# Kernel tuning notes

Hardware: AMD Instinct MI355X
Metric: run time of the kernel (lower is better)

The kernel has to match this reference:

```python
import jax, jax.numpy as jnp
import numpy as np

C_M, C_Z, C, H = 256, 128, 32, 8
EPS = 1e-5

def _ln(x, g, b):
    mu = jnp.mean(x, axis=-1, keepdims=True)
    var = jnp.var(x, axis=-1, keepdims=True)
    return (x - mu) * jax.lax.rsqrt(var + EPS) * g + b

def setup_inputs() -> dict:
    key = jax.random.key(0)
    ks = jax.random.split(key, 12)
    s = 0.02
    return {
        "m": jax.random.normal(ks[0], (128, 384, C_M), jnp.float32),
        "z": jax.random.normal(ks[1], (384, 384, C_Z), jnp.float32),
        "ln_m_g": jnp.ones((C_M,), jnp.float32),
        "ln_m_b": jnp.zeros((C_M,), jnp.float32),
        "ln_z_g": jnp.ones((C_Z,), jnp.float32),
        "ln_z_b": jnp.zeros((C_Z,), jnp.float32),
        "Wq": jax.random.normal(ks[2], (C_M, H, C), jnp.float32) * s,
        "Wk": jax.random.normal(ks[3], (C_M, H, C), jnp.float32) * s,
        "Wv": jax.random.normal(ks[4], (C_M, H, C), jnp.float32) * s,
        "Wb": jax.random.normal(ks[5], (C_Z, H), jnp.float32) * s,
        "Wg": jax.random.normal(ks[6], (C_M, H, C), jnp.float32) * s,
        "bg": jnp.ones((H, C), jnp.float32),
        "Wo": jax.random.normal(ks[7], (H, C, C_M), jnp.float32) * s,
        "bo": jnp.zeros((C_M,), jnp.float32),
    }

def reference(m, z, ln_m_g, ln_m_b, ln_z_g, ln_z_b, Wq, Wk, Wv, Wb, Wg, bg, Wo, bo):
    # Algorithm 7: MSA row-wise gated self-attention with pair bias.
    mn = _ln(m, ln_m_g, ln_m_b)                      # (S, R, c_m)
    zn = _ln(z, ln_z_g, ln_z_b)                      # (R, R, c_z)
    b = jnp.einsum('qkz,zh->hqk', zn, Wb)            # per-head pair bias (H, R, R)
    q = jnp.einsum('srm,mhc->shrc', mn, Wq)          # (S, H, R, C)
    k = jnp.einsum('srm,mhc->shrc', mn, Wk)
    v = jnp.einsum('srm,mhc->shrc', mn, Wv)
    logits = jnp.einsum('shqc,shkc->shqk', q, k) * (1.0 / np.sqrt(C)) + b[None]
    a = jax.nn.softmax(logits, axis=-1)              # (S, H, Rq, Rk)
    o = jnp.einsum('shqk,shkc->sqhc', a, v)          # (S, R, H, C)
    g = jax.nn.sigmoid(jnp.einsum('srm,mhc->srhc', mn, Wg) + bg)
    o = g * o
    out = jnp.einsum('srhc,hcm->srm', o, Wo) + bo    # (S, R, c_m)
    return out
```

## Files before the change

kernel.cpp:

```cpp
#include <hip/hip_runtime.h>
#include <hip/hip_bf16.h>

#define DEVINL __device__ __forceinline__

typedef __attribute__((ext_vector_type(8))) short bf16x8;
typedef __attribute__((ext_vector_type(4))) float f32x4;

DEVINL float bf2f(unsigned short u) {
    unsigned int v = ((unsigned int)u) << 16;
    return __builtin_bit_cast(float, v);
}
DEVINL unsigned short f2bf(float f) {
    unsigned int u = __builtin_bit_cast(unsigned int, f);
    u = (u + 0x7FFFu + ((u >> 16) & 1u)) >> 16;
    return (unsigned short)u;
}
DEVINL float wave_sum(float v) {
#pragma unroll
    for (int off = 32; off > 0; off >>= 1) v += __shfl_xor(v, off, 64);
    return v;
}
DEVINL void gload16(const void* g, void* l) {
    __builtin_amdgcn_global_load_lds(
        (const __attribute__((address_space(1))) void*)g,
        (__attribute__((address_space(3))) void*)l, 16, 0, 0);
}


__global__ __launch_bounds__(256) void k_ln_m(const float* __restrict__ m,
                                              const float* __restrict__ gm,
                                              const float* __restrict__ bm,
                                              unsigned short* __restrict__ mn) {
    const int lane = threadIdx.x & 63;
    const int row  = (blockIdx.x << 2) + (threadIdx.x >> 6);
    const float4 x = *(const float4*)(m + (size_t)row * 256 + lane * 4);
    float s  = x.x + x.y + x.z + x.w;
    float s2 = x.x * x.x + x.y * x.y + x.z * x.z + x.w * x.w;
    s = wave_sum(s); s2 = wave_sum(s2);
    const float mean = s * (1.f / 256.f);
    const float var  = s2 * (1.f / 256.f) - mean * mean;
    const float rstd = rsqrtf(var + 1e-5f);
    const float4 g = *(const float4*)(gm + lane * 4);
    const float4 b = *(const float4*)(bm + lane * 4);
    ushort4 o;
    o.x = f2bf((x.x - mean) * rstd * g.x + b.x);
    o.y = f2bf((x.y - mean) * rstd * g.y + b.y);
    o.z = f2bf((x.z - mean) * rstd * g.z + b.z);
    o.w = f2bf((x.w - mean) * rstd * g.w + b.w);
    *(ushort4*)(mn + (size_t)row * 256 + lane * 4) = o;
}

__global__ __launch_bounds__(64) void k_prep_wb(const float* __restrict__ gz,
                                                const float* __restrict__ bz,
                                                const float* __restrict__ Wb,
                                                float* __restrict__ W2,
                                                float* __restrict__ SK) {
    const int lane = threadIdx.x;
    const float LOG2E = 1.4426950408889634f;
    float sC[8], sK[8];
#pragma unroll
    for (int h = 0; h < 8; h++) { sC[h] = 0.f; sK[h] = 0.f; }
#pragma unroll
    for (int i = 0; i < 2; i++) {
        const int c = lane + i * 64;
        const float g = gz[c] * LOG2E, b = bz[c] * LOG2E;
        const float4 w0 = *(const float4*)(Wb + c * 8);
        const float4 w1 = *(const float4*)(Wb + c * 8 + 4);
        const float w[8] = {w0.x, w0.y, w0.z, w0.w, w1.x, w1.y, w1.z, w1.w};
        float wg[8];
#pragma unroll
        for (int h = 0; h < 8; h++) {
            wg[h] = g * w[h];
            sC[h] += wg[h];
            sK[h] += b * w[h];
        }
        float4 o0 = {wg[0], wg[1], wg[2], wg[3]};
        float4 o1 = {wg[4], wg[5], wg[6], wg[7]};
        *(float4*)(W2 + c * 8)     = o0;
        *(float4*)(W2 + c * 8 + 4) = o1;
    }
#pragma unroll
    for (int h = 0; h < 8; h++) { sC[h] = wave_sum(sC[h]); sK[h] = wave_sum(sK[h]); }
    if (lane == 0) {
#pragma unroll
        for (int h = 0; h < 8; h++) { SK[h] = sC[h]; SK[8 + h] = sK[h]; }
    }
}

__global__ __launch_bounds__(256) void k_ln_z_bias(const float* __restrict__ z,
                                                   const float* __restrict__ W2,
                                                   const float* __restrict__ SK,
                                                   float* __restrict__ bT) {
    const int p = blockIdx.x * 256 + threadIdx.x;
    const float* zp = z + (size_t)p * 128;

    float d[8];
#pragma unroll
    for (int h = 0; h < 8; h++) d[h] = 0.f;
    float s = 0.f, s2 = 0.f;

#pragma unroll 8
    for (int cq = 0; cq < 32; cq++) {
        const float4 zv = *(const float4*)(zp + cq * 4);
        const float za[4] = {zv.x, zv.y, zv.z, zv.w};
        s  += (zv.x + zv.y) + (zv.z + zv.w);
        s2 += (zv.x * zv.x + zv.y * zv.y) + (zv.z * zv.z + zv.w * zv.w);
#pragma unroll
        for (int cc = 0; cc < 4; cc++) {
            const float* w = W2 + (cq * 4 + cc) * 8;
#pragma unroll
            for (int h = 0; h < 8; h++) d[h] += za[cc] * w[h];
        }
    }

    const float mean = s * (1.f / 128.f);
    const float var  = s2 * (1.f / 128.f) - mean * mean;
    const float rstd = rsqrtf(var + 1e-5f);
    const float rm   = rstd * mean;

    const int q  = p / 384;
    const int kk = p - q * 384;
    const int kb = kk >> 5, kk5 = kk & 31;
    const size_t o = ((size_t)((kb * 2 + ((kk5 >> 2) & 1)) * 4 + (kk5 >> 3)) * 384 + q) * 4 + (kk5 & 3);
    float* bp = bT + o;
#pragma unroll
    for (int h = 0; h < 8; h++)
        bp[(size_t)h * 147456] = rstd * d[h] - rm * SK[h] + SK[8 + h];
}

__global__ __launch_bounds__(256) void k_prep(const float* __restrict__ S,
                                              unsigned short* __restrict__ D) {
    __shared__ float T[64][68];
    const int k0 = blockIdx.x * 64, n0 = blockIdx.y * 64;
    const int tr = threadIdx.x >> 4, tc4 = (threadIdx.x & 15) * 4;
#pragma unroll
    for (int i = 0; i < 4; i++) {
        const int k = i * 16 + tr;
        const float4 v = *(const float4*)(S + (size_t)(k0 + k) * 256 + n0 + tc4);
        T[k][tc4 + 0] = v.x; T[k][tc4 + 1] = v.y; T[k][tc4 + 2] = v.z; T[k][tc4 + 3] = v.w;
    }
    __syncthreads();
#pragma unroll
    for (int i = 0; i < 4; i++) {
        const int n = i * 16 + tr;
        ushort4 o;
        o.x = f2bf(T[tc4 + 0][n]);
        o.y = f2bf(T[tc4 + 1][n]);
        o.z = f2bf(T[tc4 + 2][n]);
        o.w = f2bf(T[tc4 + 3][n]);
        *(ushort4*)(D + (size_t)(n0 + n) * 256 + k0 + tc4) = o;
    }
}

__global__ __launch_bounds__(256) void k_prep4(const float* __restrict__ Wq,
                                               const float* __restrict__ Wk,
                                               const float* __restrict__ Wv,
                                               const float* __restrict__ Wg,
                                               unsigned short* __restrict__ D) {
    __shared__ float T[64][68];
    const int zz = blockIdx.z;
    const float* S = (zz == 0) ? Wq : (zz == 1) ? Wk : (zz == 2) ? Wv : Wg;
    unsigned short* Dz = D + (size_t)zz * 65536;
    const int k0 = blockIdx.x * 64, n0 = blockIdx.y * 64;
    const int tr = threadIdx.x >> 4, tc4 = (threadIdx.x & 15) * 4;
#pragma unroll
    for (int i = 0; i < 4; i++) {
        const int k = i * 16 + tr;
        const float4 v = *(const float4*)(S + (size_t)(k0 + k) * 256 + n0 + tc4);
        T[k][tc4 + 0] = v.x; T[k][tc4 + 1] = v.y; T[k][tc4 + 2] = v.z; T[k][tc4 + 3] = v.w;
    }
    __syncthreads();
#pragma unroll
    for (int i = 0; i < 4; i++) {
        const int n = i * 16 + tr;
        ushort4 o;
        o.x = f2bf(T[tc4 + 0][n]);
        o.y = f2bf(T[tc4 + 1][n]);
        o.z = f2bf(T[tc4 + 2][n]);
        o.w = f2bf(T[tc4 + 3][n]);
        *(ushort4*)(Dz + (size_t)(n0 + n) * 256 + k0 + tc4) = o;
    }
}

template<int MODE>
__global__ __launch_bounds__(256) void k_gemm(const unsigned short* __restrict__ A,
                                              const unsigned short* __restrict__ BT,
                                              const float* __restrict__ bias,
                                              unsigned short* __restrict__ o0,
                                              unsigned short* __restrict__ o1,
                                              unsigned short* __restrict__ o2,
                                              unsigned short* __restrict__ o3,
                                              float* __restrict__ fout) {
    __shared__ unsigned short As[8192];
    __shared__ unsigned short Bs[8192];
    const int tid = threadIdx.x;
    const int w = tid >> 6, lane = tid & 63;
    const int col = lane & 15, quad = lane >> 4;
    const int wm = w >> 1, wn = w & 1;
    const int R0 = blockIdx.x * 128;
    const int N0 = blockIdx.y * 128;

    f32x4 acc[4][4];
#pragma unroll
    for (int i = 0; i < 4; i++)
#pragma unroll
        for (int j = 0; j < 4; j++) acc[i][j] = (f32x4){0.f, 0.f, 0.f, 0.f};

    const unsigned short* Ag = A  + (size_t)R0 * 256;
    const unsigned short* Bg = BT + (size_t)N0 * 256;

    for (int ks = 0; ks < 4; ks++) {
        if (ks) __syncthreads();
        const int k0 = ks * 64;
#pragma unroll
        for (int it = 0; it < 4; it++) {
            const int cb = it * 256 + w * 64;
            const int chunk = cb + lane;
            const int row = chunk >> 3;
            const int ch  = (chunk & 7) ^ (row & 7);
            gload16(Ag + (size_t)row * 256 + k0 + ch * 8, As + (size_t)cb * 8);
            gload16(Bg + (size_t)row * 256 + k0 + ch * 8, Bs + (size_t)cb * 8);
        }
        __syncthreads();
#pragma unroll
        for (int ksub = 0; ksub < 2; ksub++) {
            const int c = ksub * 4 + quad;
            bf16x8 Af[4], Bf[4];
#pragma unroll
            for (int mt = 0; mt < 4; mt++) {
                const int r = wm * 64 + mt * 16 + col;
                Af[mt] = *(const bf16x8*)(As + r * 64 + (c ^ (r & 7)) * 8);
            }
#pragma unroll
            for (int nt = 0; nt < 4; nt++) {
                const int r = wn * 64 + nt * 16 + col;
                Bf[nt] = *(const bf16x8*)(Bs + r * 64 + (c ^ (r & 7)) * 8);
            }
#pragma unroll
            for (int mt = 0; mt < 4; mt++)
#pragma unroll
                for (int nt = 0; nt < 4; nt++)
                    acc[mt][nt] = __builtin_amdgcn_mfma_f32_16x16x32_bf16(Af[mt], Bf[nt], acc[mt][nt], 0, 0, 0);
        }
    }

    if (MODE == 0) {
        const int mat = blockIdx.y >> 1;
        const int s = R0 / 384;
        const int rbase = R0 - s * 384;
        const int n0r = (blockIdx.y & 1) * 128;
        if (mat == 1 || mat == 2) {
            unsigned short* outp = (mat == 1) ? o1 : o2;
#pragma unroll
            for (int nt = 0; nt < 4; nt++) {
                const int hc = n0r + wn * 64 + nt * 16 + col;
                const int h = hc >> 5, cc = hc & 31;
                unsigned short* op = outp + (size_t)(s * 8 + h) * 12288;
                if (mat == 1) {
#pragma unroll
                    for (int mt = 0; mt < 4; mt++) {
                        const int r2 = rbase + wm * 64 + mt * 16 + quad * 4;
                        const int ab = (r2 >> 5) * 1024 + ((r2 >> 2) & 1) * 512
                                     + ((r2 & 31) >> 3) * 128 + cc;
#pragma unroll
                        for (int rr = 0; rr < 4; rr++)
                            op[ab + rr * 32] = f2bf(acc[mt][nt][rr]);
                    }
                } else {
                    unsigned short* opv = op + (cc >> 4) * 512 + (cc & 15) * 32;
#pragma unroll
                    for (int mt = 0; mt < 4; mt++) {
                        const int r2 = rbase + wm * 64 + mt * 16 + quad * 4;
                        ushort4 o;
                        o.x = f2bf(acc[mt][nt][0]);
                        o.y = f2bf(acc[mt][nt][1]);
                        o.z = f2bf(acc[mt][nt][2]);
                        o.w = f2bf(acc[mt][nt][3]);
                        *(ushort4*)(opv + (r2 >> 5) * 1024 + (r2 & 31)) = o;
                    }
                }
            }
        } else {
            unsigned short* outp = (mat == 0) ? o0 : o3;
#pragma unroll
            for (int nt = 0; nt < 4; nt++) {
                const int hc = n0r + wn * 64 + nt * 16 + col;
                const int h = hc >> 5, cc = hc & 31;
                const float bgv = bias[hc];
                unsigned short* op = outp + (size_t)(s * 8 + h) * 384 * 32 + cc;
#pragma unroll
                for (int mt = 0; mt < 4; mt++) {
                    const int r2 = rbase + wm * 64 + mt * 16 + quad * 4;
#pragma unroll
                    for (int rr = 0; rr < 4; rr++) {
                        float v = acc[mt][nt][rr];
                        v = (mat == 3) ? 1.f / (1.f + __expf(-(v + bgv)))
                                       : v * 0.25507788224f;
                        op[(size_t)(r2 + rr) * 32] = f2bf(v);
                    }
                }
            }
        }
    } else {
#pragma unroll
        for (int nt = 0; nt < 4; nt++) {
            const int n = N0 + wn * 64 + nt * 16 + col;
            const float bov = bias[n];
            float* op = fout + n;
#pragma unroll
            for (int mt = 0; mt < 4; mt++) {
                const int r2 = R0 + wm * 64 + mt * 16 + quad * 4;
#pragma unroll
                for (int rr = 0; rr < 4; rr++)
                    op[(size_t)(r2 + rr) * 256] = acc[mt][nt][rr] + bov;
            }
        }
    }
}

__global__ __launch_bounds__(256) void k_attn(const unsigned short* __restrict__ qw,
                                              const unsigned short* __restrict__ kf,
                                              const unsigned short* __restrict__ vf,
                                              const unsigned short* __restrict__ gw,
                                              const float* __restrict__ bT,
                                              unsigned short* __restrict__ og) {
    const int s    = blockIdx.x & 127;
    const int half = (blockIdx.x >> 7) & 1;
    const int h    = blockIdx.x >> 8;
    const int tid  = threadIdx.x;
    const int wave = tid >> 6;
    const int lane = tid & 63;
    const int col  = lane & 15;
    const int quad = lane >> 4;
    const size_t base = ((size_t)(s * 8 + h)) * 12288;
    const int qbase = half * 192 + wave * 48;

    bf16x8 Qf[3];
#pragma unroll
    for (int qt = 0; qt < 3; qt++)
        Qf[qt] = *(const bf16x8*)(qw + base + (size_t)(qbase + qt * 16 + col) * 32 + quad * 8);

    f32x4 OT0[3], OT1[3];
    float lsum[3];
#pragma unroll
    for (int qt = 0; qt < 3; qt++) {
        OT0[qt] = (f32x4){0.f, 0.f, 0.f, 0.f};
        OT1[qt] = (f32x4){0.f, 0.f, 0.f, 0.f};
        lsum[qt] = 0.f;
    }

    const unsigned short* kwb = kf + base + col * 32 + quad * 8;
    const unsigned short* vtb = vf + base + col * 32 + quad * 8;
    const float* bp = bT + (size_t)h * 147456 + ((size_t)quad * 384 + qbase + col) * 4;

    for (int kb = 0; kb < 12; kb++) {
        const bf16x8 Kf0 = *(const bf16x8*)(kwb);
        const bf16x8 Kf1 = *(const bf16x8*)(kwb + 512);
        const bf16x8 VA0 = *(const bf16x8*)(vtb);
        const bf16x8 VA1 = *(const bf16x8*)(vtb + 512);
        kwb += 1024; vtb += 1024;
        f32x4 B0[3], B1[3];
#pragma unroll
        for (int qt = 0; qt < 3; qt++) {
            const float4 a = *(const float4*)(bp + qt * 64);
            const float4 b = *(const float4*)(bp + 6144 + qt * 64);
            B0[qt] = (f32x4){a.x, a.y, a.z, a.w};
            B1[qt] = (f32x4){b.x, b.y, b.z, b.w};
        }
        bp += 12288;
#pragma unroll
        for (int qt = 0; qt < 3; qt++) {
            const f32x4 St0 = __builtin_amdgcn_mfma_f32_16x16x32_bf16(Kf0, Qf[qt], B0[qt], 0, 0, 0);
            const f32x4 St1 = __builtin_amdgcn_mfma_f32_16x16x32_bf16(Kf1, Qf[qt], B1[qt], 0, 0, 0);
            float p0[4], p1[4];
            p0[0] = __builtin_amdgcn_exp2f(St0[0]);
            p0[1] = __builtin_amdgcn_exp2f(St0[1]);
            p0[2] = __builtin_amdgcn_exp2f(St0[2]);
            p0[3] = __builtin_amdgcn_exp2f(St0[3]);
            p1[0] = __builtin_amdgcn_exp2f(St1[0]);
            p1[1] = __builtin_amdgcn_exp2f(St1[1]);
            p1[2] = __builtin_amdgcn_exp2f(St1[2]);
            p1[3] = __builtin_amdgcn_exp2f(St1[3]);
            lsum[qt] += (p0[0] + p0[1]) + (p0[2] + p0[3]) + (p1[0] + p1[1]) + (p1[2] + p1[3]);
            union { bf16x8 v; __hip_bfloat162 h2[4]; } U;
            U.h2[0] = __float22bfloat162_rn(make_float2(p0[0], p0[1]));
            U.h2[1] = __float22bfloat162_rn(make_float2(p0[2], p0[3]));
            U.h2[2] = __float22bfloat162_rn(make_float2(p1[0], p1[1]));
            U.h2[3] = __float22bfloat162_rn(make_float2(p1[2], p1[3]));
            OT0[qt] = __builtin_amdgcn_mfma_f32_16x16x32_bf16(VA0, U.v, OT0[qt], 0, 0, 0);
            OT1[qt] = __builtin_amdgcn_mfma_f32_16x16x32_bf16(VA1, U.v, OT1[qt], 0, 0, 0);
        }
    }

#pragma unroll
    for (int qt = 0; qt < 3; qt++) {
        float l = lsum[qt];
        l += __shfl_xor(l, 16, 64);
        l += __shfl_xor(l, 32, 64);
        const float inv = 1.f / l;
        const int q = qbase + qt * 16 + col;
        const ushort4 g0 = *(const ushort4*)(gw + base + (size_t)q * 32 + quad * 4);
        const ushort4 g1 = *(const ushort4*)(gw + base + (size_t)q * 32 + quad * 4 + 16);
        ushort4 o0s, o1s;
        o0s.x = f2bf(OT0[qt][0] * inv * bf2f(g0.x));
        o0s.y = f2bf(OT0[qt][1] * inv * bf2f(g0.y));
        o0s.z = f2bf(OT0[qt][2] * inv * bf2f(g0.z));
        o0s.w = f2bf(OT0[qt][3] * inv * bf2f(g0.w));
        o1s.x = f2bf(OT1[qt][0] * inv * bf2f(g1.x));
        o1s.y = f2bf(OT1[qt][1] * inv * bf2f(g1.y));
        o1s.z = f2bf(OT1[qt][2] * inv * bf2f(g1.z));
        o1s.w = f2bf(OT1[qt][3] * inv * bf2f(g1.w));
        unsigned short* op = og + ((size_t)s * 384 + q) * 256 + h * 32 + quad * 4;
        *(ushort4*)(op)      = o0s;
        *(ushort4*)(op + 16) = o1s;
    }
}

extern "C" void kernel_launch(void* const* d_in, const int* in_sizes, int n_in,
                              void* d_out, int out_size, void* d_ws, size_t ws_size,
                              hipStream_t stream) {
    const float* m   = (const float*)d_in[0];
    const float* z   = (const float*)d_in[1];
    const float* lmg = (const float*)d_in[2];
    const float* lmb = (const float*)d_in[3];
    const float* lzg = (const float*)d_in[4];
    const float* lzb = (const float*)d_in[5];
    const float* Wq  = (const float*)d_in[6];
    const float* Wk  = (const float*)d_in[7];
    const float* Wv  = (const float*)d_in[8];
    const float* Wb  = (const float*)d_in[9];
    const float* Wg  = (const float*)d_in[10];
    const float* bg  = (const float*)d_in[11];
    const float* Wo  = (const float*)d_in[12];
    const float* bo  = (const float*)d_in[13];
    float* out = (float*)d_out;

    char* ws = (char*)d_ws;
    unsigned short* mn  = (unsigned short*)(ws);
    float*          bT  = (float*)(ws + 25165824);
    unsigned short* qw  = (unsigned short*)(ws + 29884416);
    unsigned short* kw  = (unsigned short*)(ws + 55050240);
    unsigned short* vw  = (unsigned short*)(ws + 80216064);
    unsigned short* gw  = (unsigned short*)(ws + 105381888);
    unsigned short* ogp = (unsigned short*)(ws + 130547712);
    unsigned short* WTp = (unsigned short*)d_out;
    float*          W2s = (float*)((char*)d_out + (1 << 20));
    float*          SKt = (float*)((char*)d_out + (1 << 20) + 4096);
    unsigned short* WoT = (unsigned short*)(ws);

    k_prep4<<<dim3(4, 4, 4), 256, 0, stream>>>(Wq, Wk, Wv, Wg, WTp);
    k_prep_wb<<<dim3(1), 64, 0, stream>>>(lzg, lzb, Wb, W2s, SKt);
    k_ln_m<<<dim3(12288), 256, 0, stream>>>(m, lmg, lmb, mn);
    k_ln_z_bias<<<dim3(576), 256, 0, stream>>>(z, W2s, SKt, bT);
    k_gemm<0><<<dim3(384, 8), 256, 0, stream>>>(mn, WTp, bg, qw, kw, vw, gw, nullptr);
    k_prep<<<dim3(4, 4), 256, 0, stream>>>(Wo, WoT);
    k_attn<<<dim3(2048), 256, 0, stream>>>(qw, kw, vw, gw, bT, ogp);
    k_gemm<1><<<dim3(384, 2), 256, 0, stream>>>(ogp, WoT, bo, nullptr, nullptr, nullptr, nullptr, out);
}
```

Before: 337.6 us.

## Pre-swizzle weights into MFMA fragment layout and double-buffer A tiles in GEMM

The weight-transpose prep kernels now write B matrices directly in MFMA fragment order, so the GEMM loads B fragments straight from global memory into registers instead of staging them through LDS. The freed LDS is used to double-buffer the A tile, prefetching the next k-slice while computing the current one and removing one barrier per iteration. The tiny Wb prep kernel is folded into the weight-prep launch as an extra grid slice, saving one launch. The cost is uncoalesced-looking direct global B reads per wave, which rely on cache reuse across blocks.

```diff
diff --git a/kernel.cpp b/kernel.cpp
--- a/kernel.cpp
+++ b/kernel.cpp
@@ -26,6 +26,14 @@
         (__attribute__((address_space(3))) void*)l, 16, 0, 0);
 }
 
+
+DEVINL void frag_store(unsigned short* D, int n, int k, ushort4 v) {
+    const int nb = n >> 7, nr = n & 127;
+    const int wn = nr >> 6, r6 = nr & 63, nt = r6 >> 4, cf = r6 & 15;
+    const int ks = k >> 6, k6 = k & 63, ksub = k6 >> 5, k5 = k6 & 31, qd = k5 >> 3, e = k5 & 7;
+    const size_t off = ((size_t)(((((nb * 4 + ks) * 2 + ksub) * 2 + wn) * 4 + nt) * 4 + qd) * 16 + cf) * 8 + e;
+    *(ushort4*)(D + off) = v;
+}
 
 __global__ __launch_bounds__(256) void k_ln_m(const float* __restrict__ m,
                                               const float* __restrict__ gm,
@@ -50,43 +58,6 @@
     *(ushort4*)(mn + (size_t)row * 256 + lane * 4) = o;
 }
 
-__global__ __launch_bounds__(64) void k_prep_wb(const float* __restrict__ gz,
-                                                const float* __restrict__ bz,
-                                                const float* __restrict__ Wb,
-                                                float* __restrict__ W2,
-                                                float* __restrict__ SK) {
-    const int lane = threadIdx.x;
-    const float LOG2E = 1.4426950408889634f;
-    float sC[8], sK[8];
-#pragma unroll
-    for (int h = 0; h < 8; h++) { sC[h] = 0.f; sK[h] = 0.f; }
-#pragma unroll
-    for (int i = 0; i < 2; i++) {
-        const int c = lane + i * 64;
-        const float g = gz[c] * LOG2E, b = bz[c] * LOG2E;
-        const float4 w0 = *(const float4*)(Wb + c * 8);
-        const float4 w1 = *(const float4*)(Wb + c * 8 + 4);
-        const float w[8] = {w0.x, w0.y, w0.z, w0.w, w1.x, w1.y, w1.z, w1.w};
-        float wg[8];
-#pragma unroll
-        for (int h = 0; h < 8; h++) {
-            wg[h] = g * w[h];
-            sC[h] += wg[h];
-            sK[h] += b * w[h];
-        }
-        float4 o0 = {wg[0], wg[1], wg[2], wg[3]};
-        float4 o1 = {wg[4], wg[5], wg[6], wg[7]};
-        *(float4*)(W2 + c * 8)     = o0;
-        *(float4*)(W2 + c * 8 + 4) = o1;
-    }
-#pragma unroll
-    for (int h = 0; h < 8; h++) { sC[h] = wave_sum(sC[h]); sK[h] = wave_sum(sK[h]); }
-    if (lane == 0) {
-#pragma unroll
-        for (int h = 0; h < 8; h++) { SK[h] = sC[h]; SK[8 + h] = sK[h]; }
-    }
-}
-
 __global__ __launch_bounds__(256) void k_ln_z_bias(const float* __restrict__ z,
                                                    const float* __restrict__ W2,
                                                    const float* __restrict__ SK,
@@ -148,7 +119,7 @@
         o.y = f2bf(T[tc4 + 1][n]);
         o.z = f2bf(T[tc4 + 2][n]);
         o.w = f2bf(T[tc4 + 3][n]);
-        *(ushort4*)(D + (size_t)(n0 + n) * 256 + k0 + tc4) = o;
+        frag_store(D, n0 + n, k0 + tc4, o);
     }
 }
 
@@ -156,7 +127,47 @@
                                                const float* __restrict__ Wk,
                                                const float* __restrict__ Wv,
                                                const float* __restrict__ Wg,
-                                               unsigned short* __restrict__ D) {
+                                               unsigned short* __restrict__ D,
+                                               const float* __restrict__ gz,
+                                               const float* __restrict__ bz,
+                                               const float* __restrict__ Wb,
+                                               float* __restrict__ W2,
+                                               float* __restrict__ SK) {
+    if (blockIdx.z == 4) {
+        if (blockIdx.x | blockIdx.y) return;
+        if (threadIdx.x >= 64) return;
+        const int lane = threadIdx.x;
+        const float LOG2E = 1.4426950408889634f;
+        float sC[8], sK[8];
+#pragma unroll
+        for (int h = 0; h < 8; h++) { sC[h] = 0.f; sK[h] = 0.f; }
+#pragma unroll
+        for (int i = 0; i < 2; i++) {
+            const int c = lane + i * 64;
+            const float g = gz[c] * LOG2E, b = bz[c] * LOG2E;
+            const float4 w0 = *(const float4*)(Wb + c * 8);
+            const float4 w1 = *(const float4*)(Wb + c * 8 + 4);
+            const float w[8] = {w0.x, w0.y, w0.z, w0.w, w1.x, w1.y, w1.z, w1.w};
+            float wg[8];
+#pragma unroll
+            for (int h = 0; h < 8; h++) {
+                wg[h] = g * w[h];
+                sC[h] += wg[h];
+                sK[h] += b * w[h];
+            }
+            float4 o0 = {wg[0], wg[1], wg[2], wg[3]};
+            float4 o1 = {wg[4], wg[5], wg[6], wg[7]};
+            *(float4*)(W2 + c * 8)     = o0;
+            *(float4*)(W2 + c * 8 + 4) = o1;
+        }
+#pragma unroll
+        for (int h = 0; h < 8; h++) { sC[h] = wave_sum(sC[h]); sK[h] = wave_sum(sK[h]); }
+        if (lane == 0) {
+#pragma unroll
+            for (int h = 0; h < 8; h++) { SK[h] = sC[h]; SK[8 + h] = sK[h]; }
+        }
+        return;
+    }
     __shared__ float T[64][68];
     const int zz = blockIdx.z;
     const float* S = (zz == 0) ? Wq : (zz == 1) ? Wk : (zz == 2) ? Wv : Wg;
@@ -178,7 +189,7 @@
         o.y = f2bf(T[tc4 + 1][n]);
         o.z = f2bf(T[tc4 + 2][n]);
         o.w = f2bf(T[tc4 + 3][n]);
-        *(ushort4*)(Dz + (size_t)(n0 + n) * 256 + k0 + tc4) = o;
+        frag_store(Dz, n0 + n, k0 + tc4, o);
     }
 }
 
@@ -191,8 +202,7 @@
                                               unsigned short* __restrict__ o2,
                                               unsigned short* __restrict__ o3,
                                               float* __restrict__ fout) {
-    __shared__ unsigned short As[8192];
-    __shared__ unsigned short Bs[8192];
+    __shared__ unsigned short As[2][8192];
     const int tid = threadIdx.x;
     const int w = tid >> 6, lane = tid & 63;
     const int col = lane & 15, quad = lane >> 4;
@@ -206,43 +216,54 @@
 #pragma unroll
         for (int j = 0; j < 4; j++) acc[i][j] = (f32x4){0.f, 0.f, 0.f, 0.f};
 
-    const unsigned short* Ag = A  + (size_t)R0 * 256;
-    const unsigned short* Bg = BT + (size_t)N0 * 256;
-
+    const unsigned short* Ag = A + (size_t)R0 * 256;
+    const unsigned short* Bg = BT + (size_t)blockIdx.y * 32768 + wn * 2048 + quad * 128 + col * 8;
+
+#define STAGE_A(ks_, buf_)                                                        \
+    {                                                                             \
+        const int k0_ = (ks_) * 64;                                               \
+        _Pragma("unroll")                                                         \
+        for (int it = 0; it < 4; it++) {                                          \
+            const int cb = it * 256 + w * 64;                                     \
+            const int chunk = cb + lane;                                          \
+            const int row = chunk >> 3;                                           \
+            const int ch  = (chunk & 7) ^ (row & 7);                              \
+            gload16(Ag + (size_t)row * 256 + k0_ + ch * 8, &As[buf_][cb * 8]);    \
+        }                                                                         \
+    }
+
+    STAGE_A(0, 0);
+    __syncthreads();
+
+#pragma unroll
     for (int ks = 0; ks < 4; ks++) {
-        if (ks) __syncthreads();
-        const int k0 = ks * 64;
-#pragma unroll
-        for (int it = 0; it < 4; it++) {
-            const int cb = it * 256 + w * 64;
-            const int chunk = cb + lane;
-            const int row = chunk >> 3;
-            const int ch  = (chunk & 7) ^ (row & 7);
-            gload16(Ag + (size_t)row * 256 + k0 + ch * 8, As + (size_t)cb * 8);
-            gload16(Bg + (size_t)row * 256 + k0 + ch * 8, Bs + (size_t)cb * 8);
-        }
-        __syncthreads();
+        const int cur = ks & 1;
+        if (ks < 3) STAGE_A(ks + 1, cur ^ 1);
+        const unsigned short* Bks = Bg + ks * 8192;
+        bf16x8 Bf0[4], Bf1[4];
+#pragma unroll
+        for (int nt = 0; nt < 4; nt++) Bf0[nt] = *(const bf16x8*)(Bks + nt * 512);
+#pragma unroll
+        for (int nt = 0; nt < 4; nt++) Bf1[nt] = *(const bf16x8*)(Bks + 4096 + nt * 512);
 #pragma unroll
         for (int ksub = 0; ksub < 2; ksub++) {
             const int c = ksub * 4 + quad;
-            bf16x8 Af[4], Bf[4];
+            bf16x8 Af[4];
 #pragma unroll
             for (int mt = 0; mt < 4; mt++) {
                 const int r = wm * 64 + mt * 16 + col;
-                Af[mt] = *(const bf16x8*)(As + r * 64 + (c ^ (r & 7)) * 8);
+                Af[mt] = *(const bf16x8*)(&As[cur][r * 64 + (c ^ (r & 7)) * 8]);
             }
 #pragma unroll
-            for (int nt = 0; nt < 4; nt++) {
-                const int r = wn * 64 + nt * 16 + col;
-                Bf[nt] = *(const bf16x8*)(Bs + r * 64 + (c ^ (r & 7)) * 8);
-            }
-#pragma unroll
             for (int mt = 0; mt < 4; mt++)
 #pragma unroll
                 for (int nt = 0; nt < 4; nt++)
-                    acc[mt][nt] = __builtin_amdgcn_mfma_f32_16x16x32_bf16(Af[mt], Bf[nt], acc[mt][nt], 0, 0, 0);
-        }
-    }
+                    acc[mt][nt] = __builtin_amdgcn_mfma_f32_16x16x32_bf16(
+                        Af[mt], ksub ? Bf1[nt] : Bf0[nt], acc[mt][nt], 0, 0, 0);
+        }
+        if (ks < 3) __syncthreads();
+    }
+#undef STAGE_A
 
     if (MODE == 0) {
         const int mat = blockIdx.y >> 1;
@@ -448,8 +469,7 @@
     float*          SKt = (float*)((char*)d_out + (1 << 20) + 4096);
     unsigned short* WoT = (unsigned short*)(ws);
 
-    k_prep4<<<dim3(4, 4, 4), 256, 0, stream>>>(Wq, Wk, Wv, Wg, WTp);
-    k_prep_wb<<<dim3(1), 64, 0, stream>>>(lzg, lzb, Wb, W2s, SKt);
+    k_prep4<<<dim3(4, 4, 5), 256, 0, stream>>>(Wq, Wk, Wv, Wg, WTp, lzg, lzb, Wb, W2s, SKt);
     k_ln_m<<<dim3(12288), 256, 0, stream>>>(m, lmg, lmb, mn);
     k_ln_z_bias<<<dim3(576), 256, 0, stream>>>(z, W2s, SKt, bT);
     k_gemm<0><<<dim3(384, 8), 256, 0, stream>>>(mn, WTp, bg, qw, kw, vw, gw, nullptr);
```

New measurement: 329.8 us. 2.3% less time.
